# Performance work log

Hardware: AMD Instinct MI355X
Metric: run time of the kernel (lower is better)

Reference implementation:

```python
import jax, jax.numpy as jnp
import numpy as np

C, CL = 64, 8
N_PTS, GRID = 250_000, 160
G2 = GRID // 2


def _build():
    """Build sparse coords and MinkowskiEngine-style kernel maps (numpy, int constants)."""
    rng = np.random.default_rng(0)
    raw = rng.integers(0, GRID, size=(int(N_PTS * 1.3), 3))
    keys = (raw[:, 0] * GRID + raw[:, 1]) * GRID + raw[:, 2]
    _, uidx = np.unique(keys, return_index=True)
    coords = raw[np.sort(uidx)][:N_PTS]
    n_in = coords.shape[0]
    # conv1: kernel 2, stride 2 -> each input voxel maps to exactly one output via one of 8 offsets
    down = coords // 2
    dkeys = (down[:, 0] * G2 + down[:, 1]) * G2 + down[:, 2]
    ukeys, inv = np.unique(dkeys, return_inverse=True)
    n_out = int(ukeys.shape[0])
    kid = (coords[:, 0] % 2) * 4 + (coords[:, 1] % 2) * 2 + (coords[:, 2] % 2)
    lists = [np.where(kid == k)[0] for k in range(8)]
    M1 = max(len(l) for l in lists)
    in1 = np.full((8, M1), n_in, np.int32)   # pad -> zero feature row
    out1 = np.full((8, M1), n_out, np.int32)  # pad -> dropped output row
    for k, l in enumerate(lists):
        in1[k, :len(l)] = l
        out1[k, :len(l)] = inv[l]
    # kernel-3, stride-1 map on the downsampled coordinate set (27 offsets)
    D = np.stack([ukeys // (G2 * G2), (ukeys // G2) % G2, ukeys % G2], 1)
    offs = [(a, b, c) for a in (-1, 0, 1) for b in (-1, 0, 1) for c in (-1, 0, 1)]
    pin, pout = [], []
    for o in offs:
        nd = D + np.array(o)
        valid = np.all((nd >= 0) & (nd < G2), 1)
        nk = (nd[:, 0] * G2 + nd[:, 1]) * G2 + nd[:, 2]
        pos = np.minimum(np.searchsorted(ukeys, nk), n_out - 1)
        found = valid & (ukeys[pos] == nk)
        ii = np.where(found)[0]
        pin.append(ii)
        pout.append(pos[ii])
    M3 = max(len(p) for p in pin)
    in3 = np.full((27, M3), n_out, np.int32)
    out3 = np.full((27, M3), n_out, np.int32)
    for k in range(27):
        in3[k, :len(pin[k])] = pin[k]
        out3[k, :len(pin[k])] = pout[k]
    return n_in, n_out, in1, out1, in3, out3


def setup_inputs() -> dict:
    n_in, n_out, in1, out1, in3, out3 = _build()
    key = jax.random.key(0)
    ks = jax.random.split(key, 16)
    s = 0.05
    return dict(
        x_F=jax.random.normal(ks[0], (n_in, C), jnp.float32),
        ctx_F=jax.random.normal(ks[1], (n_in, C), jnp.float32),
        W1=jax.random.normal(ks[2], (8, 2 * C, C), jnp.float32) * s,
        b1=jax.random.normal(ks[3], (C,), jnp.float32) * s,
        Wr00=jax.random.normal(ks[4], (27, C, C // 4), jnp.float32) * s,
        br00=jax.random.normal(ks[5], (C // 4,), jnp.float32) * s,
        Wr01=jax.random.normal(ks[6], (27, C // 4, C // 2), jnp.float32) * s,
        br01=jax.random.normal(ks[7], (C // 2,), jnp.float32) * s,
        Wr10=jax.random.normal(ks[8], (C, C // 4), jnp.float32) * s,
        br10=jax.random.normal(ks[9], (C // 4,), jnp.float32) * s,
        Wr11=jax.random.normal(ks[10], (27, C // 4, C // 4), jnp.float32) * s,
        br11=jax.random.normal(ks[11], (C // 4,), jnp.float32) * s,
        Wr12=jax.random.normal(ks[12], (C // 4, C // 2), jnp.float32) * s,
        br12=jax.random.normal(ks[13], (C // 2,), jnp.float32) * s,
        W2=jax.random.normal(ks[14], (27, C, CL), jnp.float32) * s,
        b2=jax.random.normal(ks[15], (CL,), jnp.float32) * s,
        in1=jnp.asarray(in1), out1=jnp.asarray(out1),
        in3=jnp.asarray(in3), out3=jnp.asarray(out3),
        n_out=n_out,
    )


def _sconv(F, W, b, in_idx, out_idx, n_out):
    """Kernel-map sparse conv: per-offset gather -> GEMM -> scatter-add. F:[N,Cin], W:[K,Cin,Cout]."""
    Fp = jnp.concatenate([F, jnp.zeros((1, F.shape[1]), F.dtype)], 0)
    y = jnp.zeros((n_out + 1, W.shape[2]), F.dtype)
    for k in range(W.shape[0]):  # fixed small kernel volume (8 or 27)
        y = y.at[out_idx[k]].add(Fp[in_idx[k]] @ W[k])
    return y[:n_out] + b


def reference(x_F, ctx_F, W1, b1, Wr00, br00, Wr01, br01, Wr10, br10, Wr11, br11, Wr12, br12, W2, b2, in1, out1, in3, out3, n_out):
    relu = jax.nn.relu
    f = jnp.concatenate([x_F, ctx_F], 1)               # cat(x.F, context1.F)
    h = _sconv(f, W1, b1, in1, out1, n_out)            # conv1: 2C->C, k=2, s=2
    # InceptionResNet block (PCGCv2-style)
    out0 = _sconv(relu(_sconv(h, Wr00, br00, in3, out3, n_out)), Wr01, br01, in3, out3, n_out)
    t = relu(h @ Wr10 + br10)                          # 1x1 conv
    t = relu(_sconv(t, Wr11, br11, in3, out3, n_out))  # 3x3 conv
    path1 = t @ Wr12 + br12                            # 1x1 conv
    h = jnp.concatenate([out0, path1], 1) + h          # cat + residual
    return _sconv(h, W2, b2, in3, out3, n_out)         # conv2: C->CL, k=3, s=1
```

## Files before the change

kernel.cpp:

```cpp
#include <hip/hip_runtime.h>

#define DEV __device__ __forceinline__

typedef __attribute__((ext_vector_type(8))) short bf16x8;
typedef __attribute__((ext_vector_type(4))) float f32x4;

DEV float4 ld4(const float* p){ return *reinterpret_cast<const float4*>(p); }

DEV unsigned short f2bf(float f){
    union { float f; unsigned u; } v; v.f = f;
    unsigned r = v.u + 0x7fffu + ((v.u >> 16) & 1u);
    return (unsigned short)(r >> 16);
}
DEV float bf2f(unsigned short s){
    union { unsigned u; float f; } v; v.u = ((unsigned)s) << 16;
    return v.f;
}

DEV void async16(const void* g, void* l){
    __builtin_amdgcn_global_load_lds(
        (const __attribute__((address_space(1))) unsigned*)g,
        (__attribute__((address_space(3))) unsigned*)l, 16, 0, 0);
}

DEV int xcd_swizzle(int orig, int nwg){
    int q = nwg >> 3, r = nwg & 7;
    int x = orig & 7, i = orig >> 3;
    return (x < r ? x*(q+1) : r*(q+1) + (x-r)*q) + i;
}

__global__ __launch_bounds__(256)
void inv_init(int* __restrict__ inv, long n, int defv){
    long i = (long)blockIdx.x*256 + threadIdx.x;
    if (i < n) inv[i] = defv;
}

__global__ __launch_bounds__(256)
void inv_build(const int* __restrict__ inK, const int* __restrict__ outK,
               int* __restrict__ inv, int M, int n_out){
    int k = blockIdx.y;
    int m = blockIdx.x*256 + threadIdx.x;
    if (m >= M) return;
    int o = outK[(long)k*M + m];
    if (o != n_out) inv[(long)k*n_out + o] = inK[(long)k*M + m];
}

__global__ __launch_bounds__(256)
void zero_rows(unsigned short* A, unsigned short* B, unsigned short* C,
               unsigned short* D, unsigned short* E, unsigned short* Z,
               int n_out, int n_in){
    int t = threadIdx.x;
    if (t < 64)       A[(long)n_out*64 + t] = 0;
    else if (t < 80)  B[(long)n_out*16 + (t-64)] = 0;
    else if (t < 144) C[(long)n_out*64 + (t-80)] = 0;
    else if (t < 160) D[(long)n_out*16 + (t-144)] = 0;
    else if (t < 176) E[(long)n_out*16 + (t-160)] = 0;
    else if (t < 240) Z[(long)n_in*64 + (t-176)] = 0;
}

__global__ __launch_bounds__(256)
void wfrag_unpaired(const float* __restrict__ W, unsigned short* __restrict__ F,
                    int KC, int NT, int CIN, int CR, int total){
    int idx = blockIdx.x*256 + threadIdx.x;
    if (idx >= total) return;
    int j = idx & 7, l = (idx >> 3) & 63, rest = idx >> 9;
    int nt = rest % NT, cc = rest / NT;
    int k = cc / KC, kc = cc % KC;
    int g = l >> 4, c = l & 15;
    int cin = kc*32 + g*8 + j, cout = nt*16 + c;
    float v = (cout < CR) ? W[((long)k*CIN + cin)*CR + cout] : 0.f;
    F[idx] = f2bf(v);
}

__global__ __launch_bounds__(256)
void wfrag_paired(const float* __restrict__ W, unsigned short* __restrict__ F,
                  int NKr, int NT, int CR, int total){
    int idx = blockIdx.x*256 + threadIdx.x;
    if (idx >= total) return;
    int j = idx & 7, l = (idx >> 3) & 63, rest = idx >> 9;
    int nt = rest % NT, cc = rest / NT;
    int g = l >> 4, c = l & 15;
    int koff = 2*cc + (g >> 1);
    int cin = (g & 1)*8 + j, cout = nt*16 + c;
    float v = (koff < NKr && cout < CR) ? W[((long)koff*16 + cin)*CR + cout] : 0.f;
    F[idx] = f2bf(v);
}

template<bool RELU, bool OUTBF16, int YS, int CR>
__global__ __launch_bounds__(256)
void gather27_lds(const void* __restrict__ Xv, const unsigned short* __restrict__ Wf,
                  const int* __restrict__ inv, const float* __restrict__ bias,
                  void* __restrict__ Yv, int n_out)
{
    __shared__ alignas(16) char buf[2*16384];
    const int lane = threadIdx.x & 63, w = threadIdx.x >> 6;
    const int bid = xcd_swizzle(blockIdx.x, gridDim.x);
    const long jblock = (long)bid * 128;
    if (jblock >= n_out) return;
    const int r = lane & 15, g = lane >> 4;
    const char* X = (const char*)Xv;
    const bf16x8* __restrict__ WF = (const bf16x8*)Wf;

    const int scol = (((lane & 7) ^ (lane >> 3)) << 4);
    long jr[4];
    #pragma unroll
    for (int i=0;i<4;++i)
        jr[i] = min(jblock + w*32 + i*8 + (lane >> 3), (long)n_out - 1);

    const int o00 = w*4096 + r*128 + (( 0 + g*16) ^ ((r & 7) << 4));
    const int o01 = w*4096 + r*128 + ((64 + g*16) ^ ((r & 7) << 4));
    const int o10 = o00 + 16*128;
    const int o11 = o01 + 16*128;

    f32x4 acc0 = {0,0,0,0}, acc1 = {0,0,0,0};

    int c0 = inv[jr[0]], c1 = inv[jr[1]], c2 = inv[jr[2]], c3 = inv[jr[3]];
    {
        char* d = buf + w*4096;
        async16(X + (long)c0*128 + scol, d);
        async16(X + (long)c1*128 + scol, d + 1024);
        async16(X + (long)c2*128 + scol, d + 2048);
        async16(X + (long)c3*128 + scol, d + 3072);
    }
    int n0 = inv[(long)n_out + jr[0]], n1 = inv[(long)n_out + jr[1]];
    int n2 = inv[(long)n_out + jr[2]], n3 = inv[(long)n_out + jr[3]];
    bf16x8 wc0 = WF[lane], wc1 = WF[64 + lane];
    __syncthreads();

    #pragma unroll 1
    for (int k = 0; k < 27; ++k){
        const int cb = k & 1;
        if (k < 26){
            char* d = buf + (cb^1)*16384 + w*4096;
            async16(X + (long)n0*128 + scol, d);
            async16(X + (long)n1*128 + scol, d + 1024);
            async16(X + (long)n2*128 + scol, d + 2048);
            async16(X + (long)n3*128 + scol, d + 3072);
        }
        int t0=0,t1=0,t2=0,t3=0;
        if (k < 25){
            const long ko = (long)(k+2)*n_out;
            t0 = inv[ko + jr[0]]; t1 = inv[ko + jr[1]];
            t2 = inv[ko + jr[2]]; t3 = inv[ko + jr[3]];
        }
        bf16x8 wn0 = wc0, wn1 = wc1;
        if (k < 26){
            wn0 = WF[((long)(k+1)*2    )*64 + lane];
            wn1 = WF[((long)(k+1)*2 + 1)*64 + lane];
        }
        const char* base = buf + cb*16384;
        bf16x8 a00 = *(const bf16x8*)(base + o00);
        bf16x8 a01 = *(const bf16x8*)(base + o01);
        bf16x8 a10 = *(const bf16x8*)(base + o10);
        bf16x8 a11 = *(const bf16x8*)(base + o11);
        acc0 = __builtin_amdgcn_mfma_f32_16x16x32_bf16(a00, wc0, acc0, 0, 0, 0);
        acc1 = __builtin_amdgcn_mfma_f32_16x16x32_bf16(a10, wc0, acc1, 0, 0, 0);
        acc0 = __builtin_amdgcn_mfma_f32_16x16x32_bf16(a01, wc1, acc0, 0, 0, 0);
        acc1 = __builtin_amdgcn_mfma_f32_16x16x32_bf16(a11, wc1, acc1, 0, 0, 0);
        __syncthreads();
        n0=t0; n1=t1; n2=t2; n3=t3; wc0=wn0; wc1=wn1;
    }

    const float bv = (r < CR) ? bias[r] : 0.f;
    #pragma unroll
    for (int q = 0; q < 4; ++q){
        long row = jblock + w*32 + g*4 + q;
        if (row < n_out){
            float v = acc0[q] + bv;
            if constexpr (RELU) v = fmaxf(v, 0.f);
            if constexpr (OUTBF16) ((unsigned short*)Yv)[row*YS + r] = f2bf(v);
            else if (r < CR)       ((float*)Yv)[row*YS + r] = v;
        }
        long row2 = row + 16;
        if (row2 < n_out){
            float v = acc1[q] + bv;
            if constexpr (RELU) v = fmaxf(v, 0.f);
            if constexpr (OUTBF16) ((unsigned short*)Yv)[row2*YS + r] = f2bf(v);
            else if (r < CR)       ((float*)Yv)[row2*YS + r] = v;
        }
    }
}

__global__ __launch_bounds__(256, 8)
void conv1_z(const float* __restrict__ xF, const float* __restrict__ cF,
             const unsigned short* __restrict__ Wfc1, const int* __restrict__ in1,
             unsigned short* __restrict__ Z, int M1, int n_in)
{
    __shared__ unsigned short tz[4][16*64];
    const int k = blockIdx.x;
    const int lane = threadIdx.x & 63, wave = threadIdx.x >> 6;
    const int m0 = (blockIdx.y*4 + wave)*16;
    if (m0 >= M1) return;
    const int r = lane & 15, g = lane >> 4;
    const int* __restrict__ in1k = in1 + (long)k*M1;
    const int mc = min(m0 + r, M1-1);
    const int i = in1k[mc];
    const bool valid = i < n_in;
    const long iv = valid ? i : 0;
    const bf16x8* __restrict__ WF = (const bf16x8*)(Wfc1 + (size_t)k*16*512);
    const bf16x8 az = {0,0,0,0,0,0,0,0};
    f32x4 acc[4];
    #pragma unroll
    for (int nt=0; nt<4; ++nt) acc[nt] = f32x4{0,0,0,0};

    #pragma unroll
    for (int kc=0; kc<4; ++kc){
        const float* s = (kc < 2) ? (xF + iv*64 + kc*32 + g*8)
                                  : (cF + iv*64 + (kc-2)*32 + g*8);
        float4 lo = ld4(s), hi = ld4(s+4);
        bf16x8 a;
        a[0]=(short)f2bf(lo.x); a[1]=(short)f2bf(lo.y);
        a[2]=(short)f2bf(lo.z); a[3]=(short)f2bf(lo.w);
        a[4]=(short)f2bf(hi.x); a[5]=(short)f2bf(hi.y);
        a[6]=(short)f2bf(hi.z); a[7]=(short)f2bf(hi.w);
        if (!valid) a = az;
        #pragma unroll
        for (int nt=0; nt<4; ++nt){
            bf16x8 wv = WF[((long)kc*4 + nt)*64 + lane];
            acc[nt] = __builtin_amdgcn_mfma_f32_16x16x32_bf16(a, wv, acc[nt], 0, 0, 0);
        }
    }

    #pragma unroll
    for (int q=0; q<4; ++q)
        #pragma unroll
        for (int nt=0; nt<4; ++nt)
            tz[wave][(g*4+q)*64 + nt*16 + r] = f2bf(acc[nt][q]);
    __syncthreads();
    #pragma unroll
    for (int it=0; it<2; ++it){
        int cid = it*64 + lane;
        int row = cid >> 3, c8 = (cid & 7)*8;
        int m = m0 + row;
        if (m < M1){
            int oi = in1k[m];
            long drow = (oi < n_in) ? (long)oi : (long)n_in + 1;
            *(bf16x8*)(Z + drow*64 + c8) = *(const bf16x8*)(&tz[wave][row*64 + c8]);
        }
    }
}

__global__ __launch_bounds__(256)
void conv1_sum(const unsigned short* __restrict__ Z, const int* __restrict__ inv1,
               const float* __restrict__ b1, unsigned short* __restrict__ A, int n_out)
{
    const int bid = xcd_swizzle(blockIdx.x, gridDim.x);
    const long t = (long)bid*256 + threadIdx.x;
    const long o = t >> 3;
    if (o >= n_out) return;
    const int c8 = (int)(t & 7) * 8;
    int b[8];
    #pragma unroll
    for (int k=0;k<8;++k) b[k] = inv1[(long)k*n_out + o];
    float acc[8];
    #pragma unroll
    for (int j=0;j<2;++j){
        float4 v = ld4(b1 + c8 + 4*j);
        acc[4*j]=v.x; acc[4*j+1]=v.y; acc[4*j+2]=v.z; acc[4*j+3]=v.w;
    }
    #pragma unroll
    for (int k=0;k<8;++k){
        bf16x8 z = *(const bf16x8*)(Z + (long)b[k]*64 + c8);
        #pragma unroll
        for (int j=0;j<8;++j) acc[j] += bf2f((unsigned short)z[j]);
    }
    bf16x8 outv;
    #pragma unroll
    for (int j=0;j<8;++j) outv[j] = (short)f2bf(acc[j]);
    *(bf16x8*)(A + o*64 + c8) = outv;
}

template<int NK, int G, int NT, int RB, bool RELU, int RESBASE,
         int YS, int CB, int CR, int WPE>
__global__ __launch_bounds__(256, WPE)
void mfma_g1(const void* __restrict__ Xv, const unsigned short* __restrict__ Wf,
             const int* __restrict__ inv, const float* __restrict__ bias,
             const unsigned short* __restrict__ RES, unsigned short* __restrict__ Y, int n_out)
{
    const int lane = threadIdx.x & 63, wave = threadIdx.x >> 6;
    const int jbase = (blockIdx.x*4 + wave)*32;
    if (jbase >= n_out) return;
    const int r = lane & 15, g = lane >> 4;
    const int jc0 = min(jbase + r, n_out-1), jc1 = min(jbase + 16 + r, n_out-1);
    const char* X = (const char*)Xv;
    const bf16x8* __restrict__ WF = (const bf16x8*)Wf;
    f32x4 acc0[NT], acc1[NT];
    #pragma unroll
    for (int nt=0; nt<NT; ++nt){ acc0[nt] = f32x4{0,0,0,0}; acc1[nt] = f32x4{0,0,0,0}; }

    #pragma unroll 1
    for (int g0 = 0; g0 < NK; g0 += G) {
        int b0[G], b1[G];
        #pragma unroll
        for (int kk=0; kk<G; ++kk){
            int koff = 2*(g0+kk) + (g >> 1);
            b0[kk] = inv[(long)koff*n_out + jc0];
            b1[kk] = inv[(long)koff*n_out + jc1];
        }
        #pragma unroll
        for (int kk=0; kk<G; ++kk){
            const int k = g0 + kk;
            bf16x8 a0 = *(const bf16x8*)(X + (long)b0[kk]*RB + (g&1)*16);
            bf16x8 a1 = *(const bf16x8*)(X + (long)b1[kk]*RB + (g&1)*16);
            #pragma unroll
            for (int nt=0; nt<NT; ++nt){
                bf16x8 wv = WF[((long)k*NT + nt)*64 + lane];
                acc0[nt] = __builtin_amdgcn_mfma_f32_16x16x32_bf16(a0, wv, acc0[nt], 0, 0, 0);
                acc1[nt] = __builtin_amdgcn_mfma_f32_16x16x32_bf16(a1, wv, acc1[nt], 0, 0, 0);
            }
        }
    }

    float bi[NT];
    #pragma unroll
    for (int nt=0; nt<NT; ++nt){
        int c = nt*16 + r;
        bi[nt] = (c < CR) ? bias[c] : 0.f;
    }
    #pragma unroll
    for (int q=0; q<4; ++q){
        int row = jbase + g*4 + q;
        if (row < n_out){
            #pragma unroll
            for (int nt=0; nt<NT; ++nt){
                int c = nt*16 + r;
                float v = acc0[nt][q] + bi[nt];
                if constexpr (RESBASE >= 0) v += bf2f(RES[(long)row*64 + RESBASE + c]);
                if constexpr (RELU) v = fmaxf(v, 0.f);
                Y[(long)row*YS + CB + c] = f2bf(v);
            }
        }
        int row2 = jbase + 16 + g*4 + q;
        if (row2 < n_out){
            #pragma unroll
            for (int nt=0; nt<NT; ++nt){
                int c = nt*16 + r;
                float v = acc1[nt][q] + bi[nt];
                if constexpr (RESBASE >= 0) v += bf2f(RES[(long)row2*64 + RESBASE + c]);
                if constexpr (RELU) v = fmaxf(v, 0.f);
                Y[(long)row2*YS + CB + c] = f2bf(v);
            }
        }
    }
}

template<int MODE, int NT, int RB, bool RELU, int RESBASE, int YS, int CB, int CR>
__global__ __launch_bounds__(256)
void mfma_dense(const void* __restrict__ Xv, const unsigned short* __restrict__ Wf,
                const float* __restrict__ bias, const unsigned short* __restrict__ RES,
                unsigned short* __restrict__ Y, int n_out)
{
    const int lane = threadIdx.x & 63, wave = threadIdx.x >> 6;
    const int jbase = (blockIdx.x*4 + wave)*16;
    if (jbase >= n_out) return;
    const int r = lane & 15, g = lane >> 4;
    const int jrow = jbase + r;
    const bool rowok = jrow < n_out;
    const char* X = (const char*)Xv;
    const bf16x8* __restrict__ WF = (const bf16x8*)Wf;
    const bf16x8 az = {0,0,0,0,0,0,0,0};
    f32x4 acc[NT];
    #pragma unroll
    for (int nt=0; nt<NT; ++nt) acc[nt] = f32x4{0,0,0,0};

    if constexpr (MODE == 2) {
        #pragma unroll
        for (int kc=0; kc<2; ++kc){
            bf16x8 a = az;
            if (rowok) a = *(const bf16x8*)(X + (long)jrow*RB + kc*64 + g*16);
            #pragma unroll
            for (int nt=0; nt<NT; ++nt){
                bf16x8 wv = WF[((long)kc*NT + nt)*64 + lane];
                acc[nt] = __builtin_amdgcn_mfma_f32_16x16x32_bf16(a, wv, acc[nt], 0, 0, 0);
            }
        }
    } else {
        bf16x8 a = az;
        if (rowok && g < 2) a = *(const bf16x8*)(X + (long)jrow*RB + (g&1)*16);
        #pragma unroll
        for (int nt=0; nt<NT; ++nt){
            bf16x8 wv = WF[nt*64 + lane];
            acc[nt] = __builtin_amdgcn_mfma_f32_16x16x32_bf16(a, wv, acc[nt], 0, 0, 0);
        }
    }

    float bi[NT];
    #pragma unroll
    for (int nt=0; nt<NT; ++nt){
        int c = nt*16 + r;
        bi[nt] = (c < CR) ? bias[c] : 0.f;
    }
    #pragma unroll
    for (int q=0; q<4; ++q){
        int row = jbase + g*4 + q;
        if (row < n_out){
            #pragma unroll
            for (int nt=0; nt<NT; ++nt){
                int c = nt*16 + r;
                float v = acc[nt][q] + bi[nt];
                if constexpr (RESBASE >= 0) v += bf2f(RES[(long)row*64 + RESBASE + c]);
                if constexpr (RELU) v = fmaxf(v, 0.f);
                Y[(long)row*YS + CB + c] = f2bf(v);
            }
        }
    }
}

extern "C" void kernel_launch(void* const* d_in, const int* in_sizes, int n_in_cnt,
                              void* d_out, int out_size, void* d_ws, size_t ws_size,
                              hipStream_t stream)
{
    const float* xF   = (const float*)d_in[0];
    const float* ctxF = (const float*)d_in[1];
    const float* W1   = (const float*)d_in[2];
    const float* b1   = (const float*)d_in[3];
    const float* Wr00 = (const float*)d_in[4];
    const float* br00 = (const float*)d_in[5];
    const float* Wr01 = (const float*)d_in[6];
    const float* br01 = (const float*)d_in[7];
    const float* Wr10 = (const float*)d_in[8];
    const float* br10 = (const float*)d_in[9];
    const float* Wr11 = (const float*)d_in[10];
    const float* br11 = (const float*)d_in[11];
    const float* Wr12 = (const float*)d_in[12];
    const float* br12 = (const float*)d_in[13];
    const float* W2   = (const float*)d_in[14];
    const float* b2   = (const float*)d_in[15];
    const int* in1  = (const int*)d_in[16];
    const int* out1 = (const int*)d_in[17];
    const int* in3  = (const int*)d_in[18];
    const int* out3 = (const int*)d_in[19];

    const int n_out = out_size / 8;
    const int n_in  = in_sizes[0] / 64;
    const int M1 = in_sizes[16] / 8;
    const int M3 = in_sizes[18] / 27;

    char* p = (char*)d_ws;
    int* inv3 = (int*)p;                 p += (size_t)28*n_out*4;
    int* inv1 = (int*)p;                 p += (size_t)8*n_out*4;
    unsigned short* A = (unsigned short*)p;  p += (size_t)(n_out+1)*64*2;
    unsigned short* B = (unsigned short*)p;  p += (size_t)(n_out+1)*16*2;
    unsigned short* C = (unsigned short*)p;  p += (size_t)(n_out+1)*64*2;
    unsigned short* D = (unsigned short*)p;  p += (size_t)(n_out+1)*16*2;
    unsigned short* E = (unsigned short*)p;  p += (size_t)(n_out+1)*16*2;
    unsigned short* Z = (unsigned short*)p;  p += (size_t)(n_in+2)*64*2;
    unsigned short* Wf_c1 = (unsigned short*)p;  p += (size_t)32*4*512*2;
    unsigned short* Wf_00 = (unsigned short*)p;  p += (size_t)54*512*2;
    unsigned short* Wf_2  = (unsigned short*)p;  p += (size_t)54*512*2;
    unsigned short* Wf_01 = (unsigned short*)p;  p += (size_t)14*2*512*2;
    unsigned short* Wf_11 = (unsigned short*)p;  p += (size_t)14*512*2;
    unsigned short* Wf_10 = (unsigned short*)p;  p += (size_t)2*512*2;
    unsigned short* Wf_12 = (unsigned short*)p;  p += (size_t)2*512*2;
    float* OUT = (float*)d_out;

    auto cdiv = [](long a, long b){ return (int)((a + b - 1)/b); };

    inv_init<<<cdiv((long)28*n_out,256),256,0,stream>>>(inv3, (long)28*n_out, n_out);
    inv_init<<<cdiv((long)8*n_out,256),256,0,stream>>>(inv1, (long)8*n_out, n_in);
    inv_build<<<dim3(cdiv(M3,256),27),256,0,stream>>>(in3, out3, inv3, M3, n_out);
    inv_build<<<dim3(cdiv(M1,256),8),256,0,stream>>>(in1, out1, inv1, M1, n_out);
    zero_rows<<<1,256,0,stream>>>(A, B, C, D, E, Z, n_out, n_in);

    wfrag_unpaired<<<cdiv(32*4*512,256),256,0,stream>>>(W1,   Wf_c1, 4, 4, 128, 64, 32*4*512);
    wfrag_unpaired<<<cdiv(54*512,256),  256,0,stream>>>(Wr00, Wf_00, 2, 1,  64, 16, 54*512);
    wfrag_unpaired<<<cdiv(54*512,256),  256,0,stream>>>(W2,   Wf_2,  2, 1,  64,  8, 54*512);
    wfrag_unpaired<<<cdiv(2*512,256),   256,0,stream>>>(Wr10, Wf_10, 2, 1,  64, 16, 2*512);
    wfrag_paired  <<<cdiv(14*2*512,256),256,0,stream>>>(Wr01, Wf_01, 27, 2, 32, 14*2*512);
    wfrag_paired  <<<cdiv(14*512,256),  256,0,stream>>>(Wr11, Wf_11, 27, 1, 16, 14*512);
    wfrag_paired  <<<cdiv(2*512,256),   256,0,stream>>>(Wr12, Wf_12,  1, 2, 32, 2*512);

    conv1_z<<<dim3(8,cdiv(M1,64)),256,0,stream>>>(xF, ctxF, Wf_c1, in1, Z, M1, n_in);
    conv1_sum<<<cdiv((long)8*n_out,256),256,0,stream>>>(Z, inv1, b1, A, n_out);

    const int grid_g = cdiv(n_out, 128);
    const int grid_l = cdiv(n_out, 128);
    const int grid_d = cdiv(n_out, 64);

    gather27_lds<true, true, 16, 16>
        <<<grid_l,256,0,stream>>>(A, Wf_00, inv3, br00, B, n_out);
    mfma_dense<2, 1, 128, true, -1, 16, 0, 16>
        <<<grid_d,256,0,stream>>>(A, Wf_10, br10, nullptr, D, n_out);
    mfma_g1<14,7,2, 32, false, 0, 64, 0, 32, 4>
        <<<grid_g,256,0,stream>>>(B, Wf_01, inv3, br01, A, C, n_out);
    mfma_g1<14,7,1, 32, true, -1, 16, 0, 16, 4>
        <<<grid_g,256,0,stream>>>(D, Wf_11, inv3, br11, nullptr, E, n_out);
    mfma_dense<3, 2, 32, false, 32, 64, 32, 32>
        <<<grid_d,256,0,stream>>>(E, Wf_12, br12, A, C, n_out);
    gather27_lds<false, false, 8, 8>
        <<<grid_l,256,0,stream>>>(C, Wf_2, inv3, b2, OUT, n_out);
}
```

Baseline: 262.7 us.

## Process two kernel offsets per stage in gather27 with 64-row blocks

The gather27 kernel now handles 64 output rows per block (16 per wave) instead of 128, and each pipeline stage covers two kernel offsets rather than one. That cuts the barrier-separated loop from 27 iterations to 13 plus a tail, and doubles the number of blocks for more parallelism. Separately, conv1_z issues all four float4 pairs of input loads up front before converting and running MFMA, to overlap memory latency. The cost is more index and weight registers per thread and a single accumulator chain, which serialises the MFMAs within each wave.

```diff
diff --git a/kernel.cpp b/kernel.cpp
--- a/kernel.cpp
+++ b/kernel.cpp
@@ -95,88 +95,84 @@
     __shared__ alignas(16) char buf[2*16384];
     const int lane = threadIdx.x & 63, w = threadIdx.x >> 6;
     const int bid = xcd_swizzle(blockIdx.x, gridDim.x);
-    const long jblock = (long)bid * 128;
+    const long jblock = (long)bid * 64;
     if (jblock >= n_out) return;
     const int r = lane & 15, g = lane >> 4;
     const char* X = (const char*)Xv;
     const bf16x8* __restrict__ WF = (const bf16x8*)Wf;
 
     const int scol = (((lane & 7) ^ (lane >> 3)) << 4);
-    long jr[4];
-    #pragma unroll
-    for (int i=0;i<4;++i)
-        jr[i] = min(jblock + w*32 + i*8 + (lane >> 3), (long)n_out - 1);
-
-    const int o00 = w*4096 + r*128 + (( 0 + g*16) ^ ((r & 7) << 4));
-    const int o01 = w*4096 + r*128 + ((64 + g*16) ^ ((r & 7) << 4));
-    const int o10 = o00 + 16*128;
-    const int o11 = o01 + 16*128;
-
-    f32x4 acc0 = {0,0,0,0}, acc1 = {0,0,0,0};
-
-    int c0 = inv[jr[0]], c1 = inv[jr[1]], c2 = inv[jr[2]], c3 = inv[jr[3]];
+    const long jr0 = min(jblock + w*16 +     (lane >> 3), (long)n_out - 1);
+    const long jr1 = min(jblock + w*16 + 8 + (lane >> 3), (long)n_out - 1);
+
+    const int ro0 = w*4096 + r*128 + (( 0 + g*16) ^ ((r & 7) << 4));
+    const int ro1 = w*4096 + r*128 + ((64 + g*16) ^ ((r & 7) << 4));
+
+    f32x4 acc = {0,0,0,0};
+
+    int i0a = inv[jr0],                 i0b = inv[jr1];
+    int i1a = inv[(long)n_out + jr0],   i1b = inv[(long)n_out + jr1];
     {
         char* d = buf + w*4096;
-        async16(X + (long)c0*128 + scol, d);
-        async16(X + (long)c1*128 + scol, d + 1024);
-        async16(X + (long)c2*128 + scol, d + 2048);
-        async16(X + (long)c3*128 + scol, d + 3072);
-    }
-    int n0 = inv[(long)n_out + jr[0]], n1 = inv[(long)n_out + jr[1]];
-    int n2 = inv[(long)n_out + jr[2]], n3 = inv[(long)n_out + jr[3]];
-    bf16x8 wc0 = WF[lane], wc1 = WF[64 + lane];
+        async16(X + (long)i0a*128 + scol, d);
+        async16(X + (long)i0b*128 + scol, d + 1024);
+        async16(X + (long)i1a*128 + scol, d + 2048);
+        async16(X + (long)i1b*128 + scol, d + 3072);
+    }
+    int n0a = inv[(long)2*n_out + jr0], n0b = inv[(long)2*n_out + jr1];
+    int n1a = inv[(long)3*n_out + jr0], n1b = inv[(long)3*n_out + jr1];
+    bf16x8 w00 = WF[0*64 + lane], w01 = WF[1*64 + lane];
+    bf16x8 w10 = WF[2*64 + lane], w11 = WF[3*64 + lane];
     __syncthreads();
 
     #pragma unroll 1
-    for (int k = 0; k < 27; ++k){
-        const int cb = k & 1;
-        if (k < 26){
+    for (int t = 0; t < 13; ++t){
+        const int cb = t & 1;
+        {
             char* d = buf + (cb^1)*16384 + w*4096;
-            async16(X + (long)n0*128 + scol, d);
-            async16(X + (long)n1*128 + scol, d + 1024);
-            async16(X + (long)n2*128 + scol, d + 2048);
-            async16(X + (long)n3*128 + scol, d + 3072);
-        }
-        int t0=0,t1=0,t2=0,t3=0;
-        if (k < 25){
-            const long ko = (long)(k+2)*n_out;
-            t0 = inv[ko + jr[0]]; t1 = inv[ko + jr[1]];
-            t2 = inv[ko + jr[2]]; t3 = inv[ko + jr[3]];
-        }
-        bf16x8 wn0 = wc0, wn1 = wc1;
-        if (k < 26){
-            wn0 = WF[((long)(k+1)*2    )*64 + lane];
-            wn1 = WF[((long)(k+1)*2 + 1)*64 + lane];
-        }
+            async16(X + (long)n0a*128 + scol, d);
+            async16(X + (long)n0b*128 + scol, d + 1024);
+            async16(X + (long)n1a*128 + scol, d + 2048);
+            async16(X + (long)n1b*128 + scol, d + 3072);
+        }
+        const long kiA = (long)min(2*t+4, 26) * n_out;
+        const long kiB = (long)min(2*t+5, 26) * n_out;
+        int t0a = inv[kiA + jr0], t0b = inv[kiA + jr1];
+        int t1a = inv[kiB + jr0], t1b = inv[kiB + jr1];
+        const long kwA = (long)min(2*t+2, 26) * 2;
+        const long kwB = (long)min(2*t+3, 26) * 2;
+        bf16x8 nw00 = WF[(kwA  )*64 + lane], nw01 = WF[(kwA+1)*64 + lane];
+        bf16x8 nw10 = WF[(kwB  )*64 + lane], nw11 = WF[(kwB+1)*64 + lane];
         const char* base = buf + cb*16384;
-        bf16x8 a00 = *(const bf16x8*)(base + o00);
-        bf16x8 a01 = *(const bf16x8*)(base + o01);
-        bf16x8 a10 = *(const bf16x8*)(base + o10);
-        bf16x8 a11 = *(const bf16x8*)(base + o11);
-        acc0 = __builtin_amdgcn_mfma_f32_16x16x32_bf16(a00, wc0, acc0, 0, 0, 0);
-        acc1 = __builtin_amdgcn_mfma_f32_16x16x32_bf16(a10, wc0, acc1, 0, 0, 0);
-        acc0 = __builtin_amdgcn_mfma_f32_16x16x32_bf16(a01, wc1, acc0, 0, 0, 0);
-        acc1 = __builtin_amdgcn_mfma_f32_16x16x32_bf16(a11, wc1, acc1, 0, 0, 0);
+        bf16x8 a00 = *(const bf16x8*)(base + ro0);
+        bf16x8 a01 = *(const bf16x8*)(base + ro1);
+        bf16x8 a10 = *(const bf16x8*)(base + 2048 + ro0);
+        bf16x8 a11 = *(const bf16x8*)(base + 2048 + ro1);
+        acc = __builtin_amdgcn_mfma_f32_16x16x32_bf16(a00, w00, acc, 0, 0, 0);
+        acc = __builtin_amdgcn_mfma_f32_16x16x32_bf16(a01, w01, acc, 0, 0, 0);
+        acc = __builtin_amdgcn_mfma_f32_16x16x32_bf16(a10, w10, acc, 0, 0, 0);
+        acc = __builtin_amdgcn_mfma_f32_16x16x32_bf16(a11, w11, acc, 0, 0, 0);
         __syncthreads();
-        n0=t0; n1=t1; n2=t2; n3=t3; wc0=wn0; wc1=wn1;
+        n0a=t0a; n0b=t0b; n1a=t1a; n1b=t1b;
+        w00=nw00; w01=nw01; w10=nw10; w11=nw11;
+    }
+    {
+        const char* base = buf + 16384;
+        bf16x8 a00 = *(const bf16x8*)(base + ro0);
+        bf16x8 a01 = *(const bf16x8*)(base + ro1);
+        acc = __builtin_amdgcn_mfma_f32_16x16x32_bf16(a00, w00, acc, 0, 0, 0);
+        acc = __builtin_amdgcn_mfma_f32_16x16x32_bf16(a01, w01, acc, 0, 0, 0);
     }
 
     const float bv = (r < CR) ? bias[r] : 0.f;
     #pragma unroll
     for (int q = 0; q < 4; ++q){
-        long row = jblock + w*32 + g*4 + q;
+        long row = jblock + w*16 + g*4 + q;
         if (row < n_out){
-            float v = acc0[q] + bv;
+            float v = acc[q] + bv;
             if constexpr (RELU) v = fmaxf(v, 0.f);
             if constexpr (OUTBF16) ((unsigned short*)Yv)[row*YS + r] = f2bf(v);
             else if (r < CR)       ((float*)Yv)[row*YS + r] = v;
-        }
-        long row2 = row + 16;
-        if (row2 < n_out){
-            float v = acc1[q] + bv;
-            if constexpr (RELU) v = fmaxf(v, 0.f);
-            if constexpr (OUTBF16) ((unsigned short*)Yv)[row2*YS + r] = f2bf(v);
-            else if (r < CR)       ((float*)Yv)[row2*YS + r] = v;
         }
     }
 }
@@ -203,16 +199,21 @@
     #pragma unroll
     for (int nt=0; nt<4; ++nt) acc[nt] = f32x4{0,0,0,0};
 
+    float4 lo[4], hi[4];
     #pragma unroll
     for (int kc=0; kc<4; ++kc){
         const float* s = (kc < 2) ? (xF + iv*64 + kc*32 + g*8)
                                   : (cF + iv*64 + (kc-2)*32 + g*8);
-        float4 lo = ld4(s), hi = ld4(s+4);
+        lo[kc] = ld4(s);
+        hi[kc] = ld4(s+4);
+    }
+    #pragma unroll
+    for (int kc=0; kc<4; ++kc){
         bf16x8 a;
-        a[0]=(short)f2bf(lo.x); a[1]=(short)f2bf(lo.y);
-        a[2]=(short)f2bf(lo.z); a[3]=(short)f2bf(lo.w);
-        a[4]=(short)f2bf(hi.x); a[5]=(short)f2bf(hi.y);
-        a[6]=(short)f2bf(hi.z); a[7]=(short)f2bf(hi.w);
+        a[0]=(short)f2bf(lo[kc].x); a[1]=(short)f2bf(lo[kc].y);
+        a[2]=(short)f2bf(lo[kc].z); a[3]=(short)f2bf(lo[kc].w);
+        a[4]=(short)f2bf(hi[kc].x); a[5]=(short)f2bf(hi[kc].y);
+        a[6]=(short)f2bf(hi[kc].z); a[7]=(short)f2bf(hi[kc].w);
         if (!valid) a = az;
         #pragma unroll
         for (int nt=0; nt<4; ++nt){
@@ -474,7 +475,7 @@
     conv1_sum<<<cdiv((long)8*n_out,256),256,0,stream>>>(Z, inv1, b1, A, n_out);
 
     const int grid_g = cdiv(n_out, 128);
-    const int grid_l = cdiv(n_out, 128);
+    const int grid_l = cdiv(n_out, 64);
     const int grid_d = cdiv(n_out, 64);
 
     gather27_lds<true, true, 16, 16>
```

After: 273.3 us. 1.04x slower.
